# Optimization experiments

Measured on AMD Instinct MI355X. Metric: run time of the kernel, lower is better.

The kernel has to match this reference:

```python
import jax, jax.numpy as jnp
import numpy as np

# Dims: B=256 batch, S=512 src_len, H=512 hidden, E=256 embed, V=16000 vocab, L=1 layer
B, S, H, E, V = 256, 512, 512, 256, 16000


def setup_inputs() -> dict:
    key = jax.random.key(0)
    ks = jax.random.split(key, 12)
    inp = {
        'tgt': jax.random.randint(ks[0], (B, 1), 0, V),
        'hidden': jax.random.normal(ks[1], (1, B, H), jnp.float32),
        'cell': jax.random.normal(ks[2], (1, B, H), jnp.float32),
        'encoder_outputs': jax.random.normal(ks[3], (B, S, H), jnp.float32),
        # parameters
        'emb_table': jax.random.normal(ks[4], (V, E), jnp.float32) * 0.02,
        'attn_W': jax.random.normal(ks[5], (H, 2 * H), jnp.float32) * (1.0 / np.sqrt(2 * H)),
        'attn_b': jnp.zeros((H,), jnp.float32),
        'v': jax.random.uniform(ks[6], (H,), jnp.float32, -1.0 / np.sqrt(H), 1.0 / np.sqrt(H)),
        'W_ih': jax.random.normal(ks[7], (4 * H, E + H), jnp.float32) * (1.0 / np.sqrt(H)),
        'W_hh': jax.random.normal(ks[8], (4 * H, H), jnp.float32) * (1.0 / np.sqrt(H)),
        'b_ih': jnp.zeros((4 * H,), jnp.float32),
        'b_hh': jnp.zeros((4 * H,), jnp.float32),
        'fc_W': jax.random.normal(ks[9], (V, H), jnp.float32) * (1.0 / np.sqrt(H)),
        'fc_b': jnp.zeros((V,), jnp.float32),
    }
    return inp


def reference(tgt, hidden, cell, encoder_outputs, emb_table, attn_W, attn_b, v,
              W_ih, W_hh, b_ih, b_hh, fc_W, fc_b):
    # Embedding (dropout = identity, eval mode)  -> [B, 1, E]
    embedded = emb_table[tgt]
    h = hidden[-1]                                   # [B, H]
    c = cell[-1]                                     # [B, H]

    # Bahdanau additive attention
    Sdim = encoder_outputs.shape[1]
    h_rep = jnp.broadcast_to(h[:, None, :], (h.shape[0], Sdim, h.shape[1]))
    cat = jnp.concatenate([h_rep, encoder_outputs], axis=2)          # [B, S, 2H]
    energy = jnp.tanh(jnp.einsum('bsk,hk->bsh', cat, attn_W) + attn_b)
    scores = jnp.einsum('h,bsh->bs', v, energy)                      # [B, S]
    attn = jax.nn.softmax(scores, axis=1)                            # [B, S]

    # context = bmm(attn[:,None,:], encoder_outputs)  -> [B, H]
    context = jnp.einsum('bs,bsh->bh', attn, encoder_outputs)

    # Single-step LSTM cell (PyTorch gate order i, f, g, o)
    x = jnp.concatenate([embedded[:, 0, :], context], axis=1)        # [B, E+H]
    gates = x @ W_ih.T + b_ih + h @ W_hh.T + b_hh                    # [B, 4H]
    i, f, g, o = jnp.split(gates, 4, axis=1)
    c_new = jax.nn.sigmoid(f) * c + jax.nn.sigmoid(i) * jnp.tanh(g)
    h_new = jax.nn.sigmoid(o) * jnp.tanh(c_new)

    prediction = h_new @ fc_W.T + fc_b                               # [B, V]
    return prediction, h_new[None], c_new[None], attn[:, None, :]
```

## Files before the change

kernel.cpp:

```cpp
#include <hip/hip_runtime.h>
#include <hip/hip_bf16.h>

#define B_ 256
#define S_ 512
#define H_ 512
#define E_ 256
#define V_ 16000

typedef __attribute__((ext_vector_type(4))) float f32x4_t;
typedef __attribute__((ext_vector_type(2))) float f32x2_t;
typedef __attribute__((ext_vector_type(8))) short bf16x8_t;
typedef __attribute__((ext_vector_type(2))) unsigned u32x2_t;

#define W2_SCALE 64.0f
#define W2_INV   0.015625f

__device__ __forceinline__ bf16x8_t pack8(f32x4_t a, f32x4_t b) {
    union { unsigned u[4]; bf16x8_t v; } o;
    asm("v_cvt_pk_bf16_f32 %0, %1, %2" : "=v"(o.u[0]) : "v"(a[0]), "v"(a[1]));
    asm("v_cvt_pk_bf16_f32 %0, %1, %2" : "=v"(o.u[1]) : "v"(a[2]), "v"(a[3]));
    asm("v_cvt_pk_bf16_f32 %0, %1, %2" : "=v"(o.u[2]) : "v"(b[0]), "v"(b[1]));
    asm("v_cvt_pk_bf16_f32 %0, %1, %2" : "=v"(o.u[3]) : "v"(b[2]), "v"(b[3]));
    return o.v;
}

__device__ __forceinline__ void cvt8(short* dst, const float* src) {
    f32x4_t a = *(const f32x4_t*)src;
    f32x4_t b = *(const f32x4_t*)(src + 4);
    *(bf16x8_t*)dst = pack8(a, b);
}

__device__ __forceinline__ u32x2_t f32x8_to_fp8x8(f32x4_t a, f32x4_t b, float s) {
    unsigned d0 = 0, d1 = 0;
    d0 = __builtin_amdgcn_cvt_pk_fp8_f32(a[0] * s, a[1] * s, d0, false);
    d0 = __builtin_amdgcn_cvt_pk_fp8_f32(a[2] * s, a[3] * s, d0, true);
    d1 = __builtin_amdgcn_cvt_pk_fp8_f32(b[0] * s, b[1] * s, d1, false);
    d1 = __builtin_amdgcn_cvt_pk_fp8_f32(b[2] * s, b[3] * s, d1, true);
    u32x2_t r; r[0] = d0; r[1] = d1;
    return r;
}

__device__ __forceinline__ float tanh5(float x) {
    float e = __expf(2.f * x);
    return 1.f - 2.f * __builtin_amdgcn_rcpf(e + 1.f);
}

__device__ __forceinline__ int physc(int c, int r) {
    return ((((c & 7) << 3) | (c >> 3)) ^ (r & 7));
}

__global__ void pack_w2(const float* __restrict__ attn_W, unsigned* __restrict__ Bp)
{
    const int c    = blockIdx.x * 256 + threadIdx.x;
    const int lane = c & 63;
    const int nf   = (c >> 6) & 3;
    const int wn   = (c >> 8) & 7;
    const int kk   = c >> 11;
    const int col  = wn * 64 + nf * 16 + (lane & 15);
    const int k    = kk * 32 + (lane >> 4) * 8;
    const float* src = attn_W + (size_t)col * (2 * H_) + H_ + k;
    f32x4_t a = *(const f32x4_t*)src;
    f32x4_t b = *(const f32x4_t*)(src + 4);
    *(u32x2_t*)(Bp + (size_t)c * 2) = f32x8_to_fp8x8(a, b, W2_SCALE);
}

__global__ void bias1_kernel(const float* __restrict__ hidden,
                             const float* __restrict__ attn_W,
                             const float* __restrict__ attn_b,
                             float* __restrict__ bias1)
{
    const int t  = threadIdx.x;
    const int b0 = blockIdx.x * 2;
    __shared__ float h_s[2][512];
    h_s[0][t] = hidden[(size_t)b0 * H_ + t];
    h_s[1][t] = hidden[(size_t)(b0 + 1) * H_ + t];
    __syncthreads();
    const float* wrow = attn_W + (size_t)t * (2 * H_);
    float a0 = 0.f, a1 = 0.f;
#pragma unroll 4
    for (int k = 0; k < 512; k += 4) {
        f32x4_t wv = *(const f32x4_t*)(wrow + k);
        a0 = fmaf(wv[0], h_s[0][k],     a0);
        a0 = fmaf(wv[1], h_s[0][k + 1], a0);
        a0 = fmaf(wv[2], h_s[0][k + 2], a0);
        a0 = fmaf(wv[3], h_s[0][k + 3], a0);
        a1 = fmaf(wv[0], h_s[1][k],     a1);
        a1 = fmaf(wv[1], h_s[1][k + 1], a1);
        a1 = fmaf(wv[2], h_s[1][k + 2], a1);
        a1 = fmaf(wv[3], h_s[1][k + 3], a1);
    }
    const float bb = attn_b[t];
    bias1[(size_t)b0 * H_ + t]       = a0 + bb;
    bias1[(size_t)(b0 + 1) * H_ + t] = a1 + bb;
}

__global__ void fused_attn(const float* __restrict__ enc,
                           const unsigned* __restrict__ Bp,
                           const float* __restrict__ bias1,
                           const float* __restrict__ vvec,
                           float* __restrict__ e_ws,
                           float* __restrict__ lpart,
                           float* __restrict__ ctxpart)
{
    __shared__ unsigned char buf8[32 * 512];
    __shared__ float bias_s[512];
    __shared__ float v_s[512];
    __shared__ float red[32][9];
    __shared__ float e_loc[32];

    const int t    = threadIdx.x;
    const int lane = t & 63;
    const int w    = t >> 6;
    const int b    = blockIdx.x >> 4;
    const int q    = blockIdx.x & 15;

    bias_s[t] = bias1[(size_t)b * H_ + t];
    v_s[t]    = vvec[t];

    const int srow = t >> 4;
    const int sc   = t & 15;
    const float* gp = enc + ((size_t)b * S_ + q * 32 + srow) * H_ + sc * 32;
#pragma unroll
    for (int i = 0; i < 4; ++i) {
        f32x4_t a = *(const f32x4_t*)(gp + i * 8);
        f32x4_t c = *(const f32x4_t*)(gp + i * 8 + 4);
        *(u32x2_t*)&buf8[srow * 512 + physc(sc * 4 + i, srow) * 8] =
            f32x8_to_fp8x8(a, c, 1.0f);
    }
    __syncthreads();

    const int l15 = lane & 15;
    const int hi  = lane >> 4;
    const int Y   = l15 & 7;
    const unsigned char* abase = buf8 + l15 * 512 + hi * 64;
    const unsigned* bbase = Bp + (size_t)w * 512 + lane * 2;

    f32x4_t acc[2][4];
#pragma unroll
    for (int mf = 0; mf < 2; ++mf)
#pragma unroll
        for (int nf = 0; nf < 4; ++nf)
            acc[mf][nf] = (f32x4_t){0.f, 0.f, 0.f, 0.f};

#pragma unroll
    for (int kk2 = 0; kk2 < 8; ++kk2) {
        const unsigned char* ap = abase + ((kk2 ^ Y) << 3);
        const unsigned* bp = bbase + (size_t)kk2 * 8192;
#pragma unroll
        for (int par = 0; par < 2; ++par) {
            const unsigned char* app = ap + par * 256;
            const unsigned* bpp = bp + par * 4096;
            long a0 = *(const long*)(app);
            long a1 = *(const long*)(app + 8192);
            long b0 = *(const long*)(bpp);
            long b1 = *(const long*)(bpp + 128);
            long b2 = *(const long*)(bpp + 256);
            long b3 = *(const long*)(bpp + 384);
            __builtin_amdgcn_s_setprio(1);
            acc[0][0] = __builtin_amdgcn_mfma_f32_16x16x32_fp8_fp8(a0, b0, acc[0][0], 0, 0, 0);
            acc[1][0] = __builtin_amdgcn_mfma_f32_16x16x32_fp8_fp8(a1, b0, acc[1][0], 0, 0, 0);
            acc[0][1] = __builtin_amdgcn_mfma_f32_16x16x32_fp8_fp8(a0, b1, acc[0][1], 0, 0, 0);
            acc[1][1] = __builtin_amdgcn_mfma_f32_16x16x32_fp8_fp8(a1, b1, acc[1][1], 0, 0, 0);
            acc[0][2] = __builtin_amdgcn_mfma_f32_16x16x32_fp8_fp8(a0, b2, acc[0][2], 0, 0, 0);
            acc[1][2] = __builtin_amdgcn_mfma_f32_16x16x32_fp8_fp8(a1, b2, acc[1][2], 0, 0, 0);
            acc[0][3] = __builtin_amdgcn_mfma_f32_16x16x32_fp8_fp8(a0, b3, acc[0][3], 0, 0, 0);
            acc[1][3] = __builtin_amdgcn_mfma_f32_16x16x32_fp8_fp8(a1, b3, acc[1][3], 0, 0, 0);
            __builtin_amdgcn_s_setprio(0);
        }
    }

    float part[8];
#pragma unroll
    for (int i = 0; i < 8; ++i) part[i] = 0.f;
#pragma unroll
    for (int nf = 0; nf < 4; ++nf) {
        const int col = w * 64 + nf * 16 + l15;
        const float bbv = bias_s[col];
        const float vl  = v_s[col];
#pragma unroll
        for (int mf = 0; mf < 2; ++mf)
#pragma unroll
            for (int r = 0; r < 4; ++r)
                part[mf * 4 + r] += vl * tanh5(fmaf(acc[mf][nf][r], W2_INV, bbv));
    }
#pragma unroll
    for (int i = 0; i < 8; ++i) {
        float p = part[i];
        p += __shfl_xor(p, 1);
        p += __shfl_xor(p, 2);
        p += __shfl_xor(p, 4);
        p += __shfl_xor(p, 8);
        part[i] = p;
    }
    if (l15 == 0) {
#pragma unroll
        for (int mf = 0; mf < 2; ++mf)
#pragma unroll
            for (int r = 0; r < 4; ++r)
                red[mf * 16 + (hi << 2) + r][w] = part[mf * 4 + r];
    }
    __syncthreads();

    if (t < 32) {
        float s = red[t][0] + red[t][1] + red[t][2] + red[t][3]
                + red[t][4] + red[t][5] + red[t][6] + red[t][7];
        e_loc[t] = __expf(s);
    }
    __syncthreads();

    const int cg = lane >> 3;
    const int cc = (lane & 7) * 8 + w;
    float acc8[8];
#pragma unroll
    for (int j = 0; j < 8; ++j) acc8[j] = 0.f;
#pragma unroll
    for (int i = 0; i < 4; ++i) {
        const int r   = i * 8 + cg;
        const float e = e_loc[r];
        u32x2_t ch = *(const u32x2_t*)&buf8[r * 512 + physc(cc, r) * 8];
        f32x2_t f0 = __builtin_amdgcn_cvt_pk_f32_fp8(ch[0], false);
        f32x2_t f1 = __builtin_amdgcn_cvt_pk_f32_fp8(ch[0], true);
        f32x2_t f2 = __builtin_amdgcn_cvt_pk_f32_fp8(ch[1], false);
        f32x2_t f3 = __builtin_amdgcn_cvt_pk_f32_fp8(ch[1], true);
        acc8[0] = fmaf(e, f0[0], acc8[0]);
        acc8[1] = fmaf(e, f0[1], acc8[1]);
        acc8[2] = fmaf(e, f1[0], acc8[2]);
        acc8[3] = fmaf(e, f1[1], acc8[3]);
        acc8[4] = fmaf(e, f2[0], acc8[4]);
        acc8[5] = fmaf(e, f2[1], acc8[5]);
        acc8[6] = fmaf(e, f3[0], acc8[6]);
        acc8[7] = fmaf(e, f3[1], acc8[7]);
    }
#pragma unroll
    for (int m = 8; m < 64; m <<= 1)
#pragma unroll
        for (int j = 0; j < 8; ++j)
            acc8[j] += __shfl_xor(acc8[j], m);
#pragma unroll
    for (int j = 0; j < 8; ++j)
        if (cg == j)
            ctxpart[(size_t)blockIdx.x * H_ + cc * 8 + j] = acc8[j];

    if (t < 32) {
        float sv = e_loc[t];
        sv += __shfl_xor(sv, 1);
        sv += __shfl_xor(sv, 2);
        sv += __shfl_xor(sv, 4);
        sv += __shfl_xor(sv, 8);
        sv += __shfl_xor(sv, 16);
        if (lane == 0) lpart[blockIdx.x] = sv;
        e_ws[(size_t)b * S_ + q * 32 + t] = e_loc[t];
    }
}

__global__ void combine_kernel(const float* __restrict__ e_ws,
                               const float* __restrict__ lpart,
                               const float* __restrict__ ctxpart,
                               float* __restrict__ out_attn,
                               short* __restrict__ x_cat)
{
    const int b = blockIdx.x, t = threadIdx.x;
    float l = 0.f;
#pragma unroll
    for (int j = 0; j < 16; ++j) l += lpart[16 * b + j];
    const float li = 1.f / l;
    out_attn[(size_t)b * S_ + t] = e_ws[(size_t)b * S_ + t] * li;
    float ctx = 0.f;
#pragma unroll
    for (int j = 0; j < 16; ++j)
        ctx += ctxpart[(size_t)(16 * b + j) * H_ + t];
    union { float f; unsigned u; } v; v.f = ctx * li;
    unsigned r = v.u + 0x7fffu + ((v.u >> 16) & 1u);
    x_cat[(size_t)b * 1280 + 256 + t] = (short)(r >> 16);
}

template<int KIND>
__global__ __launch_bounds__(256, 2)
void gemm_std(const short* __restrict__ Abf,
              const float* __restrict__ B0,
              const float* __restrict__ B1,
              const float* __restrict__ bias0,
              const float* __restrict__ bias1v,
              float* __restrict__ out)
{
    constexpr int K = (KIND == 0) ? 1280 : 512;
    constexpr int N = (KIND == 0) ? 2048 : 16000;

    __shared__ short As[128 * 40];
    __shared__ short Bs[128 * 40];

    const int t    = threadIdx.x;
    const int lane = t & 63;
    const int w    = t >> 6;
    const int wm   = w >> 1;
    const int wn   = w & 1;
    const int row0 = blockIdx.x * 128;
    const int col0 = blockIdx.y * 128;

    f32x4_t acc[4][4];
#pragma unroll
    for (int i = 0; i < 4; ++i)
#pragma unroll
        for (int j = 0; j < 4; ++j)
            acc[i][j] = (f32x4_t){0.f, 0.f, 0.f, 0.f};

    const int arow = t >> 1, ah = (t & 1) * 16;
    const int bcol = t >> 1, bh = (t & 1) * 16;

    for (int ks = 0; ks < K / 32; ++ks) {
        const int k0 = ks * 32;
        __syncthreads();
        const short* asrc = Abf + (size_t)(row0 + arow) * K + k0 + ah;
        *(bf16x8_t*)&As[arow * 40 + ah]     = *(const bf16x8_t*)asrc;
        *(bf16x8_t*)&As[arow * 40 + ah + 8] = *(const bf16x8_t*)(asrc + 8);
        const float* bsrc;
        if constexpr (KIND == 0) {
            const int cg = col0 + bcol;
            bsrc = (k0 < 768) ? (B0 + (size_t)cg * 768 + k0 + bh)
                              : (B1 + (size_t)cg * 512 + (k0 - 768) + bh);
        } else {
            bsrc = B0 + (size_t)(col0 + bcol) * 512 + k0 + bh;
        }
        cvt8(&Bs[bcol * 40 + bh],     bsrc);
        cvt8(&Bs[bcol * 40 + bh + 8], bsrc + 8);
        __syncthreads();

        bf16x8_t af[4], bfr[4];
        const int ka = (lane >> 4) * 8;
#pragma unroll
        for (int mf = 0; mf < 4; ++mf)
            af[mf] = *(const bf16x8_t*)&As[(wm * 64 + mf * 16 + (lane & 15)) * 40 + ka];
#pragma unroll
        for (int nf = 0; nf < 4; ++nf)
            bfr[nf] = *(const bf16x8_t*)&Bs[(wn * 64 + nf * 16 + (lane & 15)) * 40 + ka];
#pragma unroll
        for (int mf = 0; mf < 4; ++mf)
#pragma unroll
            for (int nf = 0; nf < 4; ++nf)
                acc[mf][nf] = __builtin_amdgcn_mfma_f32_16x16x32_bf16(
                    af[mf], bfr[nf], acc[mf][nf], 0, 0, 0);
    }

#pragma unroll
    for (int mf = 0; mf < 4; ++mf)
#pragma unroll
        for (int nf = 0; nf < 4; ++nf) {
            const int col  = col0 + wn * 64 + nf * 16 + (lane & 15);
            const int rowb = row0 + wm * 64 + mf * 16 + ((lane >> 4) << 2);
            float bb;
            if constexpr (KIND == 0) bb = bias0[col] + bias1v[col];
            else                     bb = bias0[col];
#pragma unroll
            for (int r = 0; r < 4; ++r)
                out[(size_t)(rowb + r) * N + col] = acc[mf][nf][r] + bb;
        }
}

__global__ void prep_kernel(const int* __restrict__ tgt,
                            const float* __restrict__ emb,
                            const float* __restrict__ hidden,
                            short* __restrict__ x_cat)
{
    const int b = blockIdx.x, t = threadIdx.x;
    const int tok = tgt[b];
    union { float f; unsigned u; } v0, v1, v2;
    v0.f = emb[(size_t)tok * E_ + t];
    v1.f = hidden[(size_t)b * H_ + t];
    v2.f = hidden[(size_t)b * H_ + 256 + t];
    unsigned r0 = v0.u + 0x7fffu + ((v0.u >> 16) & 1u);
    unsigned r1 = v1.u + 0x7fffu + ((v1.u >> 16) & 1u);
    unsigned r2 = v2.u + 0x7fffu + ((v2.u >> 16) & 1u);
    x_cat[(size_t)b * 1280 + t]             = (short)(r0 >> 16);
    x_cat[(size_t)b * 1280 + 768 + t]       = (short)(r1 >> 16);
    x_cat[(size_t)b * 1280 + 768 + 256 + t] = (short)(r2 >> 16);
}

__global__ void lstm_kernel(const float* __restrict__ gates,
                            const float* __restrict__ cell,
                            float* __restrict__ out_h,
                            float* __restrict__ out_c,
                            short* __restrict__ h_bf)
{
    const int b = blockIdx.x, t = threadIdx.x;
    const float* g = gates + (size_t)b * 2048;
    const float gi = g[t], gf = g[512 + t], gg = g[1024 + t], go = g[1536 + t];
    const float c  = cell[(size_t)b * H_ + t];
    const float si = 1.f / (1.f + __expf(-gi));
    const float sf = 1.f / (1.f + __expf(-gf));
    const float so = 1.f / (1.f + __expf(-go));
    const float cn = sf * c + si * tanhf(gg);
    const float hn = so * tanhf(cn);
    out_h[(size_t)b * H_ + t] = hn;
    out_c[(size_t)b * H_ + t] = cn;
    union { float f; unsigned u; } v; v.f = hn;
    unsigned r = v.u + 0x7fffu + ((v.u >> 16) & 1u);
    h_bf[(size_t)b * H_ + t]  = (short)(r >> 16);
}

extern "C" void kernel_launch(void* const* d_in, const int* in_sizes, int n_in,
                              void* d_out, int out_size, void* d_ws, size_t ws_size,
                              hipStream_t stream)
{
    (void)in_sizes; (void)n_in; (void)out_size; (void)ws_size;

    const int*   tgt    = (const int*)d_in[0];
    const float* hidden = (const float*)d_in[1];
    const float* cell   = (const float*)d_in[2];
    const float* enc    = (const float*)d_in[3];
    const float* emb    = (const float*)d_in[4];
    const float* attn_W = (const float*)d_in[5];
    const float* attn_b = (const float*)d_in[6];
    const float* vv     = (const float*)d_in[7];
    const float* W_ih   = (const float*)d_in[8];
    const float* W_hh   = (const float*)d_in[9];
    const float* b_ih   = (const float*)d_in[10];
    const float* b_hh   = (const float*)d_in[11];
    const float* fc_W   = (const float*)d_in[12];
    const float* fc_b   = (const float*)d_in[13];

    float* out_pred = (float*)d_out;
    float* out_h    = out_pred + (size_t)B_ * V_;
    float* out_c    = out_h + (size_t)B_ * H_;
    float* out_attn = out_c + (size_t)B_ * H_;

    char*  ws      = (char*)d_ws;
    float* bias1   = (float*)ws;
    float* gates   = bias1 + (size_t)B_ * H_;
    float* e_ws    = gates + (size_t)B_ * 2048;
    float* lpart   = e_ws + (size_t)B_ * S_;
    float* ctxpart = lpart + 4096;
    short* x_cat   = (short*)(ctxpart + (size_t)4096 * H_);
    short* h_bf    = x_cat + (size_t)B_ * 1280;
    unsigned* b2p  = (unsigned*)(h_bf + (size_t)B_ * H_);

    pack_w2<<<128, 256, 0, stream>>>(attn_W, b2p);
    prep_kernel<<<B_, 256, 0, stream>>>(tgt, emb, hidden, x_cat);
    bias1_kernel<<<128, 512, 0, stream>>>(hidden, attn_W, attn_b, bias1);
    fused_attn<<<16 * B_, 512, 0, stream>>>(enc, b2p, bias1, vv, e_ws, lpart, ctxpart);
    combine_kernel<<<B_, 512, 0, stream>>>(e_ws, lpart, ctxpart, out_attn, x_cat);
    gemm_std<0><<<dim3(2, 16), 256, 0, stream>>>(x_cat, W_ih, W_hh, b_ih, b_hh, gates);
    lstm_kernel<<<B_, 512, 0, stream>>>(gates, cell, out_h, out_c, h_bf);
    gemm_std<1><<<dim3(2, 125), 256, 0, stream>>>(h_bf, fc_W, nullptr, fc_b, nullptr, out_pred);
}
```

Measured before the change: 240.2 us.

## Split-K gates GEMM into two partial outputs and widen packed weight loads

The gates GEMM (K=1280) is split into two K halves over a third grid dimension. Each half writes its own partial gate buffer, and the LSTM kernel sums the two partials and adds both biases. This doubles the block count from 32 to 64 so more compute units are busy, at the cost of an extra partial-gate write and read. The fp8 attention-weight packing is also rearranged so each lane reads its B fragments with two 16-byte loads instead of four 8-byte loads in the attention MFMA loop.

New measurement: 201.5 us. 16.1% less time.

```diff
diff --git a/kernel.cpp b/kernel.cpp
--- a/kernel.cpp
+++ b/kernel.cpp
@@ -11,6 +11,7 @@
 typedef __attribute__((ext_vector_type(2))) float f32x2_t;
 typedef __attribute__((ext_vector_type(8))) short bf16x8_t;
 typedef __attribute__((ext_vector_type(2))) unsigned u32x2_t;
+typedef __attribute__((ext_vector_type(4))) unsigned u32x4_t;
 
 #define W2_SCALE 64.0f
 #define W2_INV   0.015625f
@@ -51,17 +52,21 @@
 
 __global__ void pack_w2(const float* __restrict__ attn_W, unsigned* __restrict__ Bp)
 {
-    const int c    = blockIdx.x * 256 + threadIdx.x;
-    const int lane = c & 63;
-    const int nf   = (c >> 6) & 3;
-    const int wn   = (c >> 8) & 7;
-    const int kk   = c >> 11;
-    const int col  = wn * 64 + nf * 16 + (lane & 15);
+    const int u    = blockIdx.x * 256 + threadIdx.x;
+    const int lane = u & 63;
+    const int p    = (u >> 6) & 1;
+    const int wn   = (u >> 7) & 7;
+    const int kk   = u >> 10;
+    const int col0 = wn * 64 + (2 * p) * 16 + (lane & 15);
     const int k    = kk * 32 + (lane >> 4) * 8;
-    const float* src = attn_W + (size_t)col * (2 * H_) + H_ + k;
-    f32x4_t a = *(const f32x4_t*)src;
-    f32x4_t b = *(const f32x4_t*)(src + 4);
-    *(u32x2_t*)(Bp + (size_t)c * 2) = f32x8_to_fp8x8(a, b, W2_SCALE);
+    const float* s0 = attn_W + (size_t)col0 * (2 * H_) + H_ + k;
+    const float* s1 = s0 + (size_t)16 * (2 * H_);
+    f32x4_t a0 = *(const f32x4_t*)s0, b0 = *(const f32x4_t*)(s0 + 4);
+    f32x4_t a1 = *(const f32x4_t*)s1, b1 = *(const f32x4_t*)(s1 + 4);
+    u32x2_t lo = f32x8_to_fp8x8(a0, b0, W2_SCALE);
+    u32x2_t hi = f32x8_to_fp8x8(a1, b1, W2_SCALE);
+    u32x4_t st; st[0] = lo[0]; st[1] = lo[1]; st[2] = hi[0]; st[3] = hi[1];
+    *(u32x4_t*)(Bp + (size_t)u * 4) = st;
 }
 
 __global__ void bias1_kernel(const float* __restrict__ hidden,
@@ -133,7 +138,7 @@
     const int hi  = lane >> 4;
     const int Y   = l15 & 7;
     const unsigned char* abase = buf8 + l15 * 512 + hi * 64;
-    const unsigned* bbase = Bp + (size_t)w * 512 + lane * 2;
+    const unsigned* bbase = Bp + (size_t)w * 512 + lane * 4;
 
     f32x4_t acc[2][4];
 #pragma unroll
@@ -152,19 +157,18 @@
             const unsigned* bpp = bp + par * 4096;
             long a0 = *(const long*)(app);
             long a1 = *(const long*)(app + 8192);
-            long b0 = *(const long*)(bpp);
-            long b1 = *(const long*)(bpp + 128);
-            long b2 = *(const long*)(bpp + 256);
-            long b3 = *(const long*)(bpp + 384);
+            union { u32x4_t v; long l[2]; } q0, q1;
+            q0.v = *(const u32x4_t*)(bpp);
+            q1.v = *(const u32x4_t*)(bpp + 256);
             __builtin_amdgcn_s_setprio(1);
-            acc[0][0] = __builtin_amdgcn_mfma_f32_16x16x32_fp8_fp8(a0, b0, acc[0][0], 0, 0, 0);
-            acc[1][0] = __builtin_amdgcn_mfma_f32_16x16x32_fp8_fp8(a1, b0, acc[1][0], 0, 0, 0);
-            acc[0][1] = __builtin_amdgcn_mfma_f32_16x16x32_fp8_fp8(a0, b1, acc[0][1], 0, 0, 0);
-            acc[1][1] = __builtin_amdgcn_mfma_f32_16x16x32_fp8_fp8(a1, b1, acc[1][1], 0, 0, 0);
-            acc[0][2] = __builtin_amdgcn_mfma_f32_16x16x32_fp8_fp8(a0, b2, acc[0][2], 0, 0, 0);
-            acc[1][2] = __builtin_amdgcn_mfma_f32_16x16x32_fp8_fp8(a1, b2, acc[1][2], 0, 0, 0);
-            acc[0][3] = __builtin_amdgcn_mfma_f32_16x16x32_fp8_fp8(a0, b3, acc[0][3], 0, 0, 0);
-            acc[1][3] = __builtin_amdgcn_mfma_f32_16x16x32_fp8_fp8(a1, b3, acc[1][3], 0, 0, 0);
+            acc[0][0] = __builtin_amdgcn_mfma_f32_16x16x32_fp8_fp8(a0, q0.l[0], acc[0][0], 0, 0, 0);
+            acc[1][0] = __builtin_amdgcn_mfma_f32_16x16x32_fp8_fp8(a1, q0.l[0], acc[1][0], 0, 0, 0);
+            acc[0][1] = __builtin_amdgcn_mfma_f32_16x16x32_fp8_fp8(a0, q0.l[1], acc[0][1], 0, 0, 0);
+            acc[1][1] = __builtin_amdgcn_mfma_f32_16x16x32_fp8_fp8(a1, q0.l[1], acc[1][1], 0, 0, 0);
+            acc[0][2] = __builtin_amdgcn_mfma_f32_16x16x32_fp8_fp8(a0, q1.l[0], acc[0][2], 0, 0, 0);
+            acc[1][2] = __builtin_amdgcn_mfma_f32_16x16x32_fp8_fp8(a1, q1.l[0], acc[1][2], 0, 0, 0);
+            acc[0][3] = __builtin_amdgcn_mfma_f32_16x16x32_fp8_fp8(a0, q1.l[1], acc[0][3], 0, 0, 0);
+            acc[1][3] = __builtin_amdgcn_mfma_f32_16x16x32_fp8_fp8(a1, q1.l[1], acc[1][3], 0, 0, 0);
             __builtin_amdgcn_s_setprio(0);
         }
     }
@@ -280,11 +284,11 @@
               const float* __restrict__ B0,
               const float* __restrict__ B1,
               const float* __restrict__ bias0,
-              const float* __restrict__ bias1v,
               float* __restrict__ out)
 {
     constexpr int K = (KIND == 0) ? 1280 : 512;
     constexpr int N = (KIND == 0) ? 2048 : 16000;
+    constexpr int KITER = (KIND == 0) ? 20 : 16;
 
     __shared__ short As[128 * 40];
     __shared__ short Bs[128 * 40];
@@ -296,6 +300,9 @@
     const int wn   = w & 1;
     const int row0 = blockIdx.x * 128;
     const int col0 = blockIdx.y * 128;
+    const int z    = (KIND == 0) ? blockIdx.z : 0;
+    const int ks0  = z * KITER;
+    float* outp    = (KIND == 0) ? out + (size_t)z * 256 * 2048 : out;
 
     f32x4_t acc[4][4];
 #pragma unroll
@@ -307,8 +314,8 @@
     const int arow = t >> 1, ah = (t & 1) * 16;
     const int bcol = t >> 1, bh = (t & 1) * 16;
 
-    for (int ks = 0; ks < K / 32; ++ks) {
-        const int k0 = ks * 32;
+    for (int ksi = 0; ksi < KITER; ++ksi) {
+        const int k0 = (ks0 + ksi) * 32;
         __syncthreads();
         const short* asrc = Abf + (size_t)(row0 + arow) * K + k0 + ah;
         *(bf16x8_t*)&As[arow * 40 + ah]     = *(const bf16x8_t*)asrc;
@@ -347,12 +354,12 @@
         for (int nf = 0; nf < 4; ++nf) {
             const int col  = col0 + wn * 64 + nf * 16 + (lane & 15);
             const int rowb = row0 + wm * 64 + mf * 16 + ((lane >> 4) << 2);
-            float bb;
-            if constexpr (KIND == 0) bb = bias0[col] + bias1v[col];
-            else                     bb = bias0[col];
-#pragma unroll
-            for (int r = 0; r < 4; ++r)
-                out[(size_t)(rowb + r) * N + col] = acc[mf][nf][r] + bb;
+#pragma unroll
+            for (int r = 0; r < 4; ++r) {
+                float v = acc[mf][nf][r];
+                if constexpr (KIND == 1) v += bias0[col];
+                outp[(size_t)(rowb + r) * N + col] = v;
+            }
         }
 }
 
@@ -375,15 +382,22 @@
     x_cat[(size_t)b * 1280 + 768 + 256 + t] = (short)(r2 >> 16);
 }
 
-__global__ void lstm_kernel(const float* __restrict__ gates,
+__global__ void lstm_kernel(const float* __restrict__ gates0,
+                            const float* __restrict__ gates1,
+                            const float* __restrict__ b_ih,
+                            const float* __restrict__ b_hh,
                             const float* __restrict__ cell,
                             float* __restrict__ out_h,
                             float* __restrict__ out_c,
                             short* __restrict__ h_bf)
 {
     const int b = blockIdx.x, t = threadIdx.x;
-    const float* g = gates + (size_t)b * 2048;
-    const float gi = g[t], gf = g[512 + t], gg = g[1024 + t], go = g[1536 + t];
+    const float* g0 = gates0 + (size_t)b * 2048;
+    const float* g1 = gates1 + (size_t)b * 2048;
+    const float gi = g0[t]        + g1[t]        + b_ih[t]        + b_hh[t];
+    const float gf = g0[512 + t]  + g1[512 + t]  + b_ih[512 + t]  + b_hh[512 + t];
+    const float gg = g0[1024 + t] + g1[1024 + t] + b_ih[1024 + t] + b_hh[1024 + t];
+    const float go = g0[1536 + t] + g1[1536 + t] + b_ih[1536 + t] + b_hh[1536 + t];
     const float c  = cell[(size_t)b * H_ + t];
     const float si = 1.f / (1.f + __expf(-gi));
     const float sf = 1.f / (1.f + __expf(-gf));
@@ -425,20 +439,21 @@
 
     char*  ws      = (char*)d_ws;
     float* bias1   = (float*)ws;
-    float* gates   = bias1 + (size_t)B_ * H_;
-    float* e_ws    = gates + (size_t)B_ * 2048;
+    float* gates01 = bias1 + (size_t)B_ * H_;
+    float* e_ws    = gates01 + (size_t)2 * B_ * 2048;
     float* lpart   = e_ws + (size_t)B_ * S_;
     float* ctxpart = lpart + 4096;
     short* x_cat   = (short*)(ctxpart + (size_t)4096 * H_);
     short* h_bf    = x_cat + (size_t)B_ * 1280;
     unsigned* b2p  = (unsigned*)(h_bf + (size_t)B_ * H_);
 
-    pack_w2<<<128, 256, 0, stream>>>(attn_W, b2p);
+    pack_w2<<<64, 256, 0, stream>>>(attn_W, b2p);
     prep_kernel<<<B_, 256, 0, stream>>>(tgt, emb, hidden, x_cat);
     bias1_kernel<<<128, 512, 0, stream>>>(hidden, attn_W, attn_b, bias1);
     fused_attn<<<16 * B_, 512, 0, stream>>>(enc, b2p, bias1, vv, e_ws, lpart, ctxpart);
     combine_kernel<<<B_, 512, 0, stream>>>(e_ws, lpart, ctxpart, out_attn, x_cat);
-    gemm_std<0><<<dim3(2, 16), 256, 0, stream>>>(x_cat, W_ih, W_hh, b_ih, b_hh, gates);
-    lstm_kernel<<<B_, 512, 0, stream>>>(gates, cell, out_h, out_c, h_bf);
-    gemm_std<1><<<dim3(2, 125), 256, 0, stream>>>(h_bf, fc_W, nullptr, fc_b, nullptr, out_pred);
-}
+    gemm_std<0><<<dim3(2, 16, 2), 256, 0, stream>>>(x_cat, W_ih, W_hh, nullptr, gates01);
+    lstm_kernel<<<B_, 512, 0, stream>>>(gates01, gates01 + (size_t)B_ * 2048,
+                                        b_ih, b_hh, cell, out_h, out_c, h_bf);
+    gemm_std<1><<<dim3(2, 125), 256, 0, stream>>>(h_bf, fc_W, nullptr, fc_b, out_pred);
+}
```
